# Kernel optimization log

Measured on AMD Instinct MI355X. Metric: run time of the kernel, lower is better.

Reference implementation:

```python
import jax, jax.numpy as jnp
import numpy as np

EPS = 1e-6   # torch pairwise_distance eps added inside the norm
MARGIN = 1.0


def setup_inputs() -> dict:
    key = jax.random.key(0)
    k1, k2 = jax.random.split(key)
    B, K, D = 4096, 1024, 128
    input_features = jax.random.normal(k1, (B, D), dtype=jnp.float32)
    centroids = jax.random.normal(k2, (K, D), dtype=jnp.float32)
    return {"input_features": input_features, "centroids": centroids}


def _mode_rows(idx, num_classes):
    # idx: [B, D] ints in [0, num_classes). Returns per-row mode [B].
    # torch.mode returns the smallest value among ties; jnp.argmax also
    # returns the first (smallest) index among ties, so behavior matches.
    B = idx.shape[0]
    counts = jnp.zeros((B, num_classes), jnp.int32)
    counts = counts.at[jnp.arange(B)[:, None], idx].add(1)
    return jnp.argmax(counts, axis=1)


def reference(input_features, centroids):
    B, D = input_features.shape
    K = centroids.shape[0]

    # [B, K, D] per-dimension squared differences (mse_loss with reduce=False)
    sq = (input_features[:, None, :] - centroids[None, :, :]) ** 2
    idx_min = jnp.argmin(sq, axis=1)  # [B, D] closest centroid per dim
    idx_max = jnp.argmax(sq, axis=1)  # [B, D] furthest centroid per dim

    positives = centroids[_mode_rows(idx_min, K)]  # [B, D]
    negatives = centroids[_mode_rows(idx_max, K)]  # [B, D]

    # triplet_margin_loss(margin=1, p=2, swap=True, reduction='mean');
    # torch adds eps inside the norm: ||a - b + eps||_2
    d_pos = jnp.linalg.norm(input_features - positives + EPS, axis=1)
    d_neg = jnp.linalg.norm(input_features - negatives + EPS, axis=1)
    d_swap = jnp.linalg.norm(positives - negatives + EPS, axis=1)
    d_neg = jnp.minimum(d_neg, d_swap)

    return jnp.mean(jnp.maximum(d_pos - d_neg + MARGIN, 0.0))
```

## Files before the change

kernel.cpp:

```cpp
#include <hip/hip_runtime.h>
#include <cstdint>

#define D 128
#define K 1024
#define NB 4096
#define BB 8
#define TK 64
#define FEPS 1e-6f

typedef unsigned long long u64;
typedef unsigned int u32;
typedef unsigned short u16;


__global__ __launch_bounds__(256) void prep_columns_kernel(
    const float* __restrict__ cen, float* __restrict__ sval,
    u16* __restrict__ shead, float* __restrict__ ext, float* __restrict__ out)
{
    __shared__ u64 keys[K];
    __shared__ u64 skeys[K];

    const int dcol = blockIdx.x;
    const int t = threadIdx.x;
    if (dcol == 0 && t == 0) out[0] = 0.0f;

    u64 my[4];
    #pragma unroll
    for (int j = 0; j < 4; ++j) {
        int k = j * 256 + t;
        float v = cen[k * D + dcol];
        u32 u = __float_as_uint(v);
        u = (u & 0x80000000u) ? ~u : (u | 0x80000000u);
        my[j] = ((u64)u << 32) | (u32)k;
        keys[k] = my[j];
    }
    __syncthreads();

    int rank0 = 0, rank1 = 0, rank2 = 0, rank3 = 0;
    #pragma unroll 8
    for (int k = 0; k < K; ++k) {
        u64 kv = keys[k];
        rank0 += (kv < my[0]) ? 1 : 0;
        rank1 += (kv < my[1]) ? 1 : 0;
        rank2 += (kv < my[2]) ? 1 : 0;
        rank3 += (kv < my[3]) ? 1 : 0;
    }
    skeys[rank0] = my[0];
    skeys[rank1] = my[1];
    skeys[rank2] = my[2];
    skeys[rank3] = my[3];
    __syncthreads();

    #pragma unroll
    for (int j = 0; j < 4; ++j) {
        int p = j * 256 + t;
        u64 kp = skeys[p];
        u32 vb = (u32)(kp >> 32);
        int p0 = p;
        while (p0 > 0 && (u32)(skeys[p0 - 1] >> 32) == vb) --p0;
        int head = (int)(skeys[p0] & 1023u);
        u32 u = (vb & 0x80000000u) ? (vb & 0x7FFFFFFFu) : ~vb;
        float v = __uint_as_float(u);
        sval[dcol * K + p] = v;
        shead[dcol * K + p] = (u16)head;
        if (p == 0)     { ext[dcol]     = v; ((int*)ext)[2 * D + dcol] = head; }
        if (p == K - 1) { ext[D + dcol] = v; ((int*)ext)[3 * D + dcol] = head; }
    }
}

__global__ __launch_bounds__(256) void search_kernel(
    const float* __restrict__ x, const float* __restrict__ sval,
    const u16* __restrict__ shead, u16* __restrict__ iminT)
{
    __shared__ float svs[K];
    __shared__ u16 shs[K];

    const int col = blockIdx.x & (D - 1);
    const int chunk = blockIdx.x >> 7;
    const int t = threadIdx.x;

    ((float4*)svs)[t] = ((const float4*)(sval + col * K))[t];
    ((uint2*)shs)[t]  = ((const uint2*)(shead + col * K))[t];
    __syncthreads();

    const int b0 = chunk * 1024;
    float xq[4];
    #pragma unroll
    for (int j = 0; j < 4; ++j)
        xq[j] = x[(size_t)(b0 + j * 256 + t) * D + col];

    int pos[4];
    #pragma unroll
    for (int r = 0; r < 4; ++r) pos[r] = -1;
    #pragma unroll
    for (int s = K; s >= 1; s >>= 1) {
        #pragma unroll
        for (int r = 0; r < 4; ++r) {
            int cand = pos[r] + s;
            int cc = cand > K - 1 ? K - 1 : cand;
            float v = svs[cc];
            if (cand <= K - 1 && v <= xq[r]) pos[r] = cand;
        }
    }
    #pragma unroll
    for (int r = 0; r < 4; ++r) {
        int p1 = pos[r], p2 = pos[r] + 1;
        int c1 = p1 < 0 ? 0 : p1;
        int c2 = p2 > K - 1 ? K - 1 : p2;
        float v1 = svs[c1], v2 = svs[c2];
        int h1 = shs[c1], h2 = shs[c2];
        float d1 = xq[r] - v1, d2 = xq[r] - v2;
        float s1 = d1 * d1, s2 = d2 * d2;
        if (p1 < 0) s1 = 3.4e38f;
        if (p2 > K - 1) s2 = 3.4e38f;
        int idx;
        if (s1 < s2) idx = h1;
        else if (s2 < s1) idx = h2;
        else idx = h1 < h2 ? h1 : h2;
        iminT[(size_t)col * NB + b0 + r * 256 + t] = (u16)idx;
    }
}

__global__ __launch_bounds__(256) void mode_loss_kernel(
    const float* __restrict__ x, const float* __restrict__ cen,
    const u16* __restrict__ iminT, const float* __restrict__ ext,
    float* __restrict__ out)
{
    __shared__ float xs[BB * D];
    __shared__ u32 cntA[BB * K / 4];
    __shared__ u32 cntB[BB * K / 4];
    __shared__ int modes[2 * BB];

    const int t = threadIdx.x;
    const int b0 = blockIdx.x * BB;

    ((float4*)xs)[t] = ((const float4*)(x + (size_t)b0 * D))[t];
    {
        uint4 z = make_uint4(0u, 0u, 0u, 0u);
        uint4* a4 = (uint4*)cntA;
        uint4* b4 = (uint4*)cntB;
        #pragma unroll
        for (int j = 0; j < 2; ++j) { a4[t + 256 * j] = z; b4[t + 256 * j] = z; }
    }
    __syncthreads();

    {
        const int dd = t >> 1, half = t & 1;
        uint2 w = *(const uint2*)(iminT + (size_t)dd * NB + b0 + half * 4);
        int i0 = (int)(w.x & 0xFFFFu), i1 = (int)(w.x >> 16);
        int i2 = (int)(w.y & 0xFFFFu), i3 = (int)(w.y >> 16);
        const int rr = half * 4;
        atomicAdd(&cntA[((rr + 0) << 8) + (i0 >> 2)], 1u << ((i0 & 3) * 8));
        atomicAdd(&cntA[((rr + 1) << 8) + (i1 >> 2)], 1u << ((i1 & 3) * 8));
        atomicAdd(&cntA[((rr + 2) << 8) + (i2 >> 2)], 1u << ((i2 & 3) * 8));
        atomicAdd(&cntA[((rr + 3) << 8) + (i3 >> 2)], 1u << ((i3 & 3) * 8));
    }

    const int d = t & (D - 1);
    const int g = t >> 7;
    {
        float cminv = ext[d], cmaxv = ext[D + d];
        int cmini = ((const int*)ext)[2 * D + d];
        int cmaxi = ((const int*)ext)[3 * D + d];
        #pragma unroll
        for (int r = 0; r < 4; ++r) {
            float xv = xs[(g * 4 + r) * D + d];
            float d1 = xv - cminv;
            float d2 = xv - cmaxv;
            float s1 = d1 * d1, s2 = d2 * d2;
            int idx;
            if (s1 > s2) idx = cmini;
            else if (s2 > s1) idx = cmaxi;
            else idx = (cmini < cmaxi) ? cmini : cmaxi;
            const int rr = g * 4 + r;
            atomicAdd(&cntB[(rr << 8) + (idx >> 2)], 1u << ((idx & 3) * 8));
        }
    }
    __syncthreads();

    const int row = t >> 5;
    const int lane = t & 31;
    {
        u32 bkeyA = 0u, bkeyB = 0u;
        #pragma unroll
        for (int j = 0; j < 8; ++j) {
            const int w = j * 32 + lane;
            u32 wA = cntA[(row << 8) + w];
            u32 wB = cntB[(row << 8) + w];
            #pragma unroll
            for (int sub = 0; sub < 4; ++sub) {
                const u32 idx = (u32)(w * 4 + sub);
                u32 cA = (wA >> (sub * 8)) & 0xFFu;
                u32 cB = (wB >> (sub * 8)) & 0xFFu;
                u32 kA = (cA << 10) | (1023u - idx);
                u32 kB = (cB << 10) | (1023u - idx);
                bkeyA = kA > bkeyA ? kA : bkeyA;
                bkeyB = kB > bkeyB ? kB : bkeyB;
            }
        }
        #pragma unroll
        for (int m = 16; m >= 1; m >>= 1) {
            u32 oA = __shfl_xor(bkeyA, m);
            u32 oB = __shfl_xor(bkeyB, m);
            bkeyA = oA > bkeyA ? oA : bkeyA;
            bkeyB = oB > bkeyB ? oB : bkeyB;
        }
        if (lane == 0) {
            modes[row]      = 1023 - (int)(bkeyA & 1023u);
            modes[BB + row] = 1023 - (int)(bkeyB & 1023u);
        }
    }
    __syncthreads();

    {
        int pm = modes[row];
        int nm = modes[BB + row];
        const float* pr = cen + (size_t)pm * D;
        const float* nr = cen + (size_t)nm * D;
        float a1 = 0.f, a2 = 0.f, a3 = 0.f;
        #pragma unroll
        for (int j = 0; j < 4; ++j) {
            int dd = j * 32 + lane;
            float xv = xs[row * D + dd];
            float pv = pr[dd], nv = nr[dd];
            float e1 = xv - pv + FEPS;
            float e2 = xv - nv + FEPS;
            float e3 = pv - nv + FEPS;
            a1 += e1 * e1; a2 += e2 * e2; a3 += e3 * e3;
        }
        #pragma unroll
        for (int m = 16; m >= 1; m >>= 1) {
            a1 += __shfl_xor(a1, m);
            a2 += __shfl_xor(a2, m);
            a3 += __shfl_xor(a3, m);
        }
        if (lane == 0) {
            float dp = sqrtf(a1);
            float dneg = fminf(sqrtf(a2), sqrtf(a3));
            float term = dp - dneg + 1.0f;
            if (term > 0.f) atomicAdd(out, term * (1.0f / NB));
        }
    }
}

__global__ __launch_bounds__(256) void col_extremes_kernel(
    const float* __restrict__ cen, float* __restrict__ ws)
{
    __shared__ float mv[256]; __shared__ int mi[256];
    __shared__ float Mv[256]; __shared__ int Mi[256];
    const int dcol = blockIdx.x;
    const int t = threadIdx.x;

    float lminv = 3.4e38f; int lmini = 0;
    float lmaxv = -3.4e38f; int lmaxi = 0;
    #pragma unroll
    for (int j = 0; j < 4; ++j) {
        int k = t * 4 + j;
        float v = cen[k * D + dcol];
        if (v < lminv) { lminv = v; lmini = k; }
        if (v > lmaxv) { lmaxv = v; lmaxi = k; }
    }
    mv[t] = lminv; mi[t] = lmini; Mv[t] = lmaxv; Mi[t] = lmaxi;
    __syncthreads();
    for (int s = 128; s > 0; s >>= 1) {
        if (t < s) {
            float ov = mv[t + s]; int oi = mi[t + s];
            if (ov < mv[t] || (ov == mv[t] && oi < mi[t])) { mv[t] = ov; mi[t] = oi; }
            float Ov = Mv[t + s]; int Oi = Mi[t + s];
            if (Ov > Mv[t] || (Ov == Mv[t] && Oi < Mi[t])) { Mv[t] = Ov; Mi[t] = Oi; }
        }
        __syncthreads();
    }
    if (t == 0) {
        ws[dcol]     = mv[0];
        ws[D + dcol] = Mv[0];
        ((int*)ws)[2 * D + dcol] = mi[0];
        ((int*)ws)[3 * D + dcol] = Mi[0];
    }
}

__global__ __launch_bounds__(256) void cluster_triplet_kernel(
    const float* __restrict__ x, const float* __restrict__ cen,
    const float* __restrict__ ws, float* __restrict__ out)
{
    __shared__ float ctile[TK * D];
    __shared__ float xs[BB * D];
    __shared__ u16 imin[BB * D];
    __shared__ u16 imax[BB * D];
    __shared__ int modes[2 * BB];

    const int t = threadIdx.x;
    const int b0 = blockIdx.x * BB;

    ((float4*)xs)[t] = ((const float4*)(x + (size_t)b0 * D))[t];
    __syncthreads();

    const int d = t & (D - 1);
    const int g = t >> 7;

    float xr[4];
    #pragma unroll
    for (int r = 0; r < 4; ++r) xr[r] = xs[(g * 4 + r) * D + d];

    float best[4]; int bidx[4];
    #pragma unroll
    for (int r = 0; r < 4; ++r) { best[r] = 3.4e38f; bidx[r] = 0; }

    for (int kt = 0; kt < K / TK; ++kt) {
        __syncthreads();
        {
            const float4* src = (const float4*)(cen + (size_t)kt * TK * D);
            float4* dst = (float4*)ctile;
            #pragma unroll
            for (int j = 0; j < 8; ++j) dst[t + 256 * j] = src[t + 256 * j];
        }
        __syncthreads();
        #pragma unroll 8
        for (int kk = 0; kk < TK; ++kk) {
            float cv = ctile[kk * D + d];
            int kg = kt * TK + kk;
            #pragma unroll
            for (int r = 0; r < 4; ++r) {
                float ad = fabsf(xr[r] - cv);
                if (ad < best[r]) { best[r] = ad; bidx[r] = kg; }
            }
        }
    }

    #pragma unroll
    for (int r = 0; r < 4; ++r) imin[(g * 4 + r) * D + d] = (u16)bidx[r];

    {
        float cminv = ws[d], cmaxv = ws[D + d];
        int cmini = ((const int*)ws)[2 * D + d];
        int cmaxi = ((const int*)ws)[3 * D + d];
        #pragma unroll
        for (int r = 0; r < 4; ++r) {
            float d1 = xr[r] - cminv;
            float d2 = xr[r] - cmaxv;
            float s1 = d1 * d1, s2 = d2 * d2;
            int idx;
            if (s1 > s2) idx = cmini;
            else if (s2 > s1) idx = cmaxi;
            else idx = (cmini < cmaxi) ? cmini : cmaxi;
            imax[(g * 4 + r) * D + d] = (u16)idx;
        }
    }
    __syncthreads();

    u32* counts = (u32*)ctile;
    const int row = t >> 5;
    const int lane = t & 31;
    for (int pass = 0; pass < 2; ++pass) {
        {
            uint4* cz = (uint4*)counts;
            uint4 z = make_uint4(0u, 0u, 0u, 0u);
            #pragma unroll
            for (int j = 0; j < 8; ++j) cz[t + 256 * j] = z;
        }
        __syncthreads();
        const u16* src = (pass == 0) ? imin : imax;
        #pragma unroll
        for (int r = 0; r < 4; ++r) {
            int rr = g * 4 + r;
            atomicAdd(&counts[rr * K + (int)src[rr * D + d]], 1u);
        }
        __syncthreads();
        u32 bkey = 0u;
        for (int j = 0; j < 32; ++j) {
            int idx = j * 32 + lane;
            u32 cnt = counts[row * K + idx];
            u32 key = (cnt << 10) | (1023u - (u32)idx);
            bkey = (key > bkey) ? key : bkey;
        }
        #pragma unroll
        for (int m = 16; m >= 1; m >>= 1) {
            u32 o = __shfl_xor(bkey, m);
            bkey = (o > bkey) ? o : bkey;
        }
        if (lane == 0) modes[pass * BB + row] = 1023 - (int)(bkey & 1023u);
        __syncthreads();
    }

    {
        int pm = modes[0 * BB + row];
        int nm = modes[1 * BB + row];
        const float* pr = cen + (size_t)pm * D;
        const float* nr = cen + (size_t)nm * D;
        float a1 = 0.f, a2 = 0.f, a3 = 0.f;
        #pragma unroll
        for (int j = 0; j < 4; ++j) {
            int dd = j * 32 + lane;
            float xv = xs[row * D + dd];
            float pv = pr[dd], nv = nr[dd];
            float e1 = xv - pv + FEPS;
            float e2 = xv - nv + FEPS;
            float e3 = pv - nv + FEPS;
            a1 += e1 * e1; a2 += e2 * e2; a3 += e3 * e3;
        }
        #pragma unroll
        for (int m = 16; m >= 1; m >>= 1) {
            a1 += __shfl_xor(a1, m);
            a2 += __shfl_xor(a2, m);
            a3 += __shfl_xor(a3, m);
        }
        if (lane == 0) {
            float dp = sqrtf(a1);
            float dneg = fminf(sqrtf(a2), sqrtf(a3));
            float term = dp - dneg + 1.0f;
            if (term > 0.f) atomicAdd(out, term * (1.0f / NB));
        }
    }
}

extern "C" void kernel_launch(void* const* d_in, const int* in_sizes, int n_in,
                              void* d_out, int out_size, void* d_ws, size_t ws_size,
                              hipStream_t stream) {
    (void)in_sizes; (void)n_in; (void)out_size;
    const float* x   = (const float*)d_in[0];
    const float* cen = (const float*)d_in[1];
    float* out = (float*)d_out;

    const size_t need = (size_t)D * K * 4
                      + (size_t)D * K * 2
                      + (size_t)D * NB * 2
                      + (size_t)4 * D * 4;
    if (ws_size >= need) {
        float* sval = (float*)d_ws;
        u16* shead  = (u16*)(sval + D * K);
        u16* iminT  = shead + D * K;
        float* ext  = (float*)(iminT + (size_t)D * NB);
        prep_columns_kernel<<<D, 256, 0, stream>>>(cen, sval, shead, ext, out);
        search_kernel<<<D * (NB / 1024), 256, 0, stream>>>(x, sval, shead, iminT);
        mode_loss_kernel<<<NB / BB, 256, 0, stream>>>(x, cen, iminT, ext, out);
    } else {
        float* ws = (float*)d_ws;
        hipMemsetAsync(d_out, 0, sizeof(float), stream);
        col_extremes_kernel<<<D, 256, 0, stream>>>(cen, ws);
        cluster_triplet_kernel<<<NB / BB, 256, 0, stream>>>(x, cen, ws, out);
    }
}
```

Measured before the change: 116.9 us.

## Fuse column sort and binary search into one kernel, keep sorted columns in LDS

Merges the per-column centroid rank-sort kernel and the binary-search kernel into a single 512-thread kernel per column. The sorted values and heads stay in shared memory instead of round-tripping through global workspace, which removes one launch and the global write/read. The rank counting now uses vectorized 128-bit LDS reads. The trade-off is that only 128 blocks run the search, which was previously spread over 512 blocks, so the search phase has less parallelism.

```diff
diff --git a/kernel.cpp b/kernel.cpp
--- a/kernel.cpp
+++ b/kernel.cpp
@@ -13,47 +13,54 @@
 typedef unsigned short u16;
 
 
-__global__ __launch_bounds__(256) void prep_columns_kernel(
-    const float* __restrict__ cen, float* __restrict__ sval,
-    u16* __restrict__ shead, float* __restrict__ ext, float* __restrict__ out)
+__global__ __launch_bounds__(512) void prep_search_kernel(
+    const float* __restrict__ cen, const float* __restrict__ x,
+    u16* __restrict__ iminT, float* __restrict__ ext, float* __restrict__ out)
 {
     __shared__ u64 keys[K];
     __shared__ u64 skeys[K];
+    __shared__ float svs[K];
+    __shared__ u16 shs[K];
 
     const int dcol = blockIdx.x;
     const int t = threadIdx.x;
     if (dcol == 0 && t == 0) out[0] = 0.0f;
 
-    u64 my[4];
+    u64 my0, my1;
+    {
+        float v0 = cen[t * D + dcol];
+        float v1 = cen[(t + 512) * D + dcol];
+        u32 u0 = __float_as_uint(v0), u1 = __float_as_uint(v1);
+        u0 = (u0 & 0x80000000u) ? ~u0 : (u0 | 0x80000000u);
+        u1 = (u1 & 0x80000000u) ? ~u1 : (u1 | 0x80000000u);
+        my0 = ((u64)u0 << 32) | (u32)t;
+        my1 = ((u64)u1 << 32) | (u32)(t + 512);
+        keys[t] = my0;
+        keys[t + 512] = my1;
+    }
+    __syncthreads();
+
+    int r0 = 0, r1 = 0;
+    #pragma unroll 2
+    for (int k0 = 0; k0 < K; k0 += 8) {
+        ulonglong2 p0 = *(ulonglong2*)&keys[k0];
+        ulonglong2 p1 = *(ulonglong2*)&keys[k0 + 2];
+        ulonglong2 p2 = *(ulonglong2*)&keys[k0 + 4];
+        ulonglong2 p3 = *(ulonglong2*)&keys[k0 + 6];
+        u64 kv[8] = { p0.x, p0.y, p1.x, p1.y, p2.x, p2.y, p3.x, p3.y };
+        #pragma unroll
+        for (int j = 0; j < 8; ++j) {
+            r0 += (kv[j] < my0) ? 1 : 0;
+            r1 += (kv[j] < my1) ? 1 : 0;
+        }
+    }
+    skeys[r0] = my0;
+    skeys[r1] = my1;
+    __syncthreads();
+
     #pragma unroll
-    for (int j = 0; j < 4; ++j) {
-        int k = j * 256 + t;
-        float v = cen[k * D + dcol];
-        u32 u = __float_as_uint(v);
-        u = (u & 0x80000000u) ? ~u : (u | 0x80000000u);
-        my[j] = ((u64)u << 32) | (u32)k;
-        keys[k] = my[j];
-    }
-    __syncthreads();
-
-    int rank0 = 0, rank1 = 0, rank2 = 0, rank3 = 0;
-    #pragma unroll 8
-    for (int k = 0; k < K; ++k) {
-        u64 kv = keys[k];
-        rank0 += (kv < my[0]) ? 1 : 0;
-        rank1 += (kv < my[1]) ? 1 : 0;
-        rank2 += (kv < my[2]) ? 1 : 0;
-        rank3 += (kv < my[3]) ? 1 : 0;
-    }
-    skeys[rank0] = my[0];
-    skeys[rank1] = my[1];
-    skeys[rank2] = my[2];
-    skeys[rank3] = my[3];
-    __syncthreads();
-
-    #pragma unroll
-    for (int j = 0; j < 4; ++j) {
-        int p = j * 256 + t;
+    for (int j = 0; j < 2; ++j) {
+        int p = j * 512 + t;
         u64 kp = skeys[p];
         u32 vb = (u32)(kp >> 32);
         int p0 = p;
@@ -61,63 +68,51 @@
         int head = (int)(skeys[p0] & 1023u);
         u32 u = (vb & 0x80000000u) ? (vb & 0x7FFFFFFFu) : ~vb;
         float v = __uint_as_float(u);
-        sval[dcol * K + p] = v;
-        shead[dcol * K + p] = (u16)head;
+        svs[p] = v;
+        shs[p] = (u16)head;
         if (p == 0)     { ext[dcol]     = v; ((int*)ext)[2 * D + dcol] = head; }
         if (p == K - 1) { ext[D + dcol] = v; ((int*)ext)[3 * D + dcol] = head; }
     }
-}
-
-__global__ __launch_bounds__(256) void search_kernel(
-    const float* __restrict__ x, const float* __restrict__ sval,
-    const u16* __restrict__ shead, u16* __restrict__ iminT)
-{
-    __shared__ float svs[K];
-    __shared__ u16 shs[K];
-
-    const int col = blockIdx.x & (D - 1);
-    const int chunk = blockIdx.x >> 7;
-    const int t = threadIdx.x;
-
-    ((float4*)svs)[t] = ((const float4*)(sval + col * K))[t];
-    ((uint2*)shs)[t]  = ((const uint2*)(shead + col * K))[t];
-    __syncthreads();
-
-    const int b0 = chunk * 1024;
-    float xq[4];
-    #pragma unroll
-    for (int j = 0; j < 4; ++j)
-        xq[j] = x[(size_t)(b0 + j * 256 + t) * D + col];
-
-    int pos[4];
-    #pragma unroll
-    for (int r = 0; r < 4; ++r) pos[r] = -1;
-    #pragma unroll
-    for (int s = K; s >= 1; s >>= 1) {
+    __syncthreads();
+
+    #pragma unroll 1
+    for (int ph = 0; ph < 2; ++ph) {
+        const int b0 = ph * 2048;
+        float xq[4];
+        #pragma unroll
+        for (int j = 0; j < 4; ++j)
+            xq[j] = x[(size_t)(b0 + j * 512 + t) * D + dcol];
+
+        int pos[4];
+        #pragma unroll
+        for (int r = 0; r < 4; ++r) pos[r] = -1;
+        #pragma unroll
+        for (int s = K; s >= 1; s >>= 1) {
+            #pragma unroll
+            for (int r = 0; r < 4; ++r) {
+                int cand = pos[r] + s;
+                int cc = cand > K - 1 ? K - 1 : cand;
+                float v = svs[cc];
+                if (cand <= K - 1 && v <= xq[r]) pos[r] = cand;
+            }
+        }
         #pragma unroll
         for (int r = 0; r < 4; ++r) {
-            int cand = pos[r] + s;
-            int cc = cand > K - 1 ? K - 1 : cand;
-            float v = svs[cc];
-            if (cand <= K - 1 && v <= xq[r]) pos[r] = cand;
-        }
-    }
-    #pragma unroll
-    for (int r = 0; r < 4; ++r) {
-        int p1 = pos[r], p2 = pos[r] + 1;
-        int c1 = p1 < 0 ? 0 : p1;
-        int c2 = p2 > K - 1 ? K - 1 : p2;
-        float v1 = svs[c1], v2 = svs[c2];
-        int h1 = shs[c1], h2 = shs[c2];
-        float d1 = xq[r] - v1, d2 = xq[r] - v2;
-        float s1 = d1 * d1, s2 = d2 * d2;
-        if (p1 < 0) s1 = 3.4e38f;
-        if (p2 > K - 1) s2 = 3.4e38f;
-        int idx;
-        if (s1 < s2) idx = h1;
-        else if (s2 < s1) idx = h2;
-        else idx = h1 < h2 ? h1 : h2;
-        iminT[(size_t)col * NB + b0 + r * 256 + t] = (u16)idx;
+            int p1 = pos[r], p2 = pos[r] + 1;
+            int c1 = p1 < 0 ? 0 : p1;
+            int c2 = p2 > K - 1 ? K - 1 : p2;
+            float v1 = svs[c1], v2 = svs[c2];
+            int h1 = shs[c1], h2 = shs[c2];
+            float d1 = xq[r] - v1, d2 = xq[r] - v2;
+            float s1 = d1 * d1, s2 = d2 * d2;
+            if (p1 < 0) s1 = 3.4e38f;
+            if (p2 > K - 1) s2 = 3.4e38f;
+            int idx;
+            if (s1 < s2) idx = h1;
+            else if (s2 < s1) idx = h2;
+            else idx = h1 < h2 ? h1 : h2;
+            iminT[(size_t)dcol * NB + b0 + r * 512 + t] = (u16)idx;
+        }
     }
 }
 
@@ -421,17 +416,12 @@
     const float* cen = (const float*)d_in[1];
     float* out = (float*)d_out;
 
-    const size_t need = (size_t)D * K * 4
-                      + (size_t)D * K * 2
-                      + (size_t)D * NB * 2
+    const size_t need = (size_t)D * NB * 2
                       + (size_t)4 * D * 4;
     if (ws_size >= need) {
-        float* sval = (float*)d_ws;
-        u16* shead  = (u16*)(sval + D * K);
-        u16* iminT  = shead + D * K;
+        u16* iminT  = (u16*)d_ws;
         float* ext  = (float*)(iminT + (size_t)D * NB);
-        prep_columns_kernel<<<D, 256, 0, stream>>>(cen, sval, shead, ext, out);
-        search_kernel<<<D * (NB / 1024), 256, 0, stream>>>(x, sval, shead, iminT);
+        prep_search_kernel<<<D, 512, 0, stream>>>(cen, x, iminT, ext, out);
         mode_loss_kernel<<<NB / BB, 256, 0, stream>>>(x, cen, iminT, ext, out);
     } else {
         float* ws = (float*)d_ws;
```

Measured after the change: 114.4 us. -2.1%, faster.
